# Kernel tuning notes

Measured on AMD Instinct MI355X. Metric: run time of the kernel, lower is better.

The kernel has to match this reference:

```python
import jax, jax.numpy as jnp
import numpy as np


def _jac_det(u):
    # u: [B, 3, D, H, W] displacement field in [-1, 1]-normalized coords
    B, C, D, H, W = u.shape
    scale = jnp.array([(D - 1) / 2.0, (H - 1) / 2.0, (W - 1) / 2.0], dtype=u.dtype)
    phi = u * scale[None, :, None, None, None]
    px, py, pz = phi[:, 0], phi[:, 1], phi[:, 2]  # each [B, D, H, W]
    # torch.gradient == numpy.gradient: central differences interior, one-sided edges
    gx = lambda a: jnp.gradient(a, axis=-3)
    gy = lambda a: jnp.gradient(a, axis=-2)
    gz = lambda a: jnp.gradient(a, axis=-1)
    dxx = gx(px) + 1.0
    dxy = gy(px)
    dxz = gz(px)
    dyx = gx(py)
    dyy = gy(py) + 1.0
    dyz = gz(py)
    dzx = gx(pz)
    dzy = gy(pz)
    dzz = gz(pz) + 1.0
    det = (dxx * (dyy * dzz - dyz * dzy)
           + dxy * (dyz * dzx - dyx * dzz)
           + dxz * (dyx * dzy - dyy * dzx))
    return det


def setup_inputs() -> dict:
    key = jax.random.key(0)
    displacement_field = jax.random.normal(key, (2, 3, 160, 192, 160), dtype=jnp.float32) * 0.05
    return {"displacement_field": displacement_field}


def reference(displacement_field):
    det = _jac_det(displacement_field)
    # loss = mean(relu(-det))
    return jnp.mean(jax.nn.relu(-det))
```

## Files before the change

### kernel.cpp

```cpp
#include <hip/hip_runtime.h>

#define Dd 160
#define Hh 192
#define Ww 160
#define HW (Hh * Ww)
#define DHW ((size_t)Dd * HW)
#define NVOX_D 9830400.0

#define TH 8
#define TD 5
#define QROW (Ww / 4)
#define TPB (QROW * TH)
#define NHT (Hh / TH)
#define NDS (Dd / TD)
#define GRID1 (2 * NHT * NDS)
#define NXCD 8
#define CHUNK (GRID1 / NXCD)
#define NWAVE (TPB / 64)
#define BLK2 512

__device__ __forceinline__ float4 ld4(const float* p) {
    return *reinterpret_cast<const float4*>(p);
}

__device__ __forceinline__ float4 wgrad(float4 cc, float lft, float rgt, int w0) {
    float4 g;
    g.x = (w0 == 0)      ? (cc.y - cc.x) : 0.5f * (cc.y - lft);
    g.y = 0.5f * (cc.z - cc.x);
    g.z = 0.5f * (cc.w - cc.y);
    g.w = (w0 + 4 == Ww) ? (cc.w - cc.z) : 0.5f * (rgt - cc.z);
    return g;
}

__device__ __forceinline__ float relu_negdet(
    float gd0, float gh0, float gw0,
    float gd1, float gh1, float gw1,
    float gd2, float gh2, float gw2)
{
    const float sx = 79.5f;
    const float sy = 95.5f;
    const float sz = 79.5f;
    float dxx = fmaf(sx, gd0, 1.0f);
    float dxy = sx * gh0;
    float dxz = sx * gw0;
    float dyx = sy * gd1;
    float dyy = fmaf(sy, gh1, 1.0f);
    float dyz = sy * gw1;
    float dzx = sz * gd2;
    float dzy = sz * gh2;
    float dzz = fmaf(sz, gw2, 1.0f);
    float det = dxx * (dyy * dzz - dyz * dzy)
              + dxy * (dyz * dzx - dyx * dzz)
              + dxz * (dyx * dzy - dyy * dzx);
    return fmaxf(-det, 0.0f);
}

__global__ __launch_bounds__(TPB) void jac_partial(const float* __restrict__ u,
                                                   float* __restrict__ part)
{
    const int lg  = (blockIdx.x % NXCD) * CHUNK + blockIdx.x / NXCD;
    const int ds  = lg % NDS;
    const int ht  = (lg / NDS) % NHT;
    const int b   = lg / (NDS * NHT);

    const int tid = threadIdx.x;
    const int wq  = tid % QROW;
    const int hh  = tid / QROW;
    const int h   = ht * TH + hh;
    const int w0  = wq * 4;

    const int hm = (h > 0)      ? h - 1 : 0;
    const int hp = (h < Hh - 1) ? h + 1 : Hh - 1;
    const float hinv = 1.0f / (float)(hp - hm);
    const int offm = (hm - h) * Ww;
    const int offp = (hp - h) * Ww;

    const int d0     = ds * TD;
    const int dir    = (ds & 1) ? -1 : 1;
    const int dstart = (dir > 0) ? d0 : d0 + TD - 1;

    const float* pcA = u + (size_t)(b * 3 + 0) * DHW + (size_t)h * Ww + w0;
    const float* pcB = pcA + DHW;
    const float* pcC = pcA + 2 * DHW;

    float4 a0, a1, b0, b1, c0, c1;
    {
        int db = dstart - dir;
        db = (db < 0) ? 0 : ((db > Dd - 1) ? Dd - 1 : db);
        const size_t om = (size_t)db * HW;
        const size_t oc = (size_t)dstart * HW;
        a0 = ld4(pcA + om);  a1 = ld4(pcA + oc);
        b0 = ld4(pcB + om);  b1 = ld4(pcB + oc);
        c0 = ld4(pcC + om);  c1 = ld4(pcC + oc);
    }

    float acc = 0.0f;

    #pragma unroll
    for (int i = 0; i < TD; ++i) {
        const int d  = dstart + dir * i;
        int dn = d + dir;
        dn = (dn < 0) ? 0 : ((dn > Dd - 1) ? Dd - 1 : dn);
        const float dinvs = (float)dir * ((d > 0 && d < Dd - 1) ? 0.5f : 1.0f);
        const size_t od  = (size_t)d  * HW;
        const size_t odn = (size_t)dn * HW;

        float4 a2 = ld4(pcA + odn);
        float4 b2 = ld4(pcB + odn);
        float4 c2 = ld4(pcC + odn);

        const float* pdA = pcA + od;
        const float* pdB = pcB + od;
        const float* pdC = pcC + od;

        float4 rAm = ld4(pdA + offm), rAp = ld4(pdA + offp);
        float4 rBm = ld4(pdB + offm), rBp = ld4(pdB + offp);
        float4 rCm = ld4(pdC + offm), rCp = ld4(pdC + offp);

        float lA = (w0 > 0) ? pdA[-1] : 0.0f;
        float lB = (w0 > 0) ? pdB[-1] : 0.0f;
        float lC = (w0 > 0) ? pdC[-1] : 0.0f;
        float rA = (w0 + 4 < Ww) ? pdA[4] : 0.0f;
        float rB = (w0 + 4 < Ww) ? pdB[4] : 0.0f;
        float rC = (w0 + 4 < Ww) ? pdC[4] : 0.0f;

        float4 gwA = wgrad(a1, lA, rA, w0);
        float4 gwB = wgrad(b1, lB, rB, w0);
        float4 gwC = wgrad(c1, lC, rC, w0);

        float4 ghA = make_float4((rAp.x - rAm.x) * hinv, (rAp.y - rAm.y) * hinv,
                                 (rAp.z - rAm.z) * hinv, (rAp.w - rAm.w) * hinv);
        float4 ghB = make_float4((rBp.x - rBm.x) * hinv, (rBp.y - rBm.y) * hinv,
                                 (rBp.z - rBm.z) * hinv, (rBp.w - rBm.w) * hinv);
        float4 ghC = make_float4((rCp.x - rCm.x) * hinv, (rCp.y - rCm.y) * hinv,
                                 (rCp.z - rCm.z) * hinv, (rCp.w - rCm.w) * hinv);

        float4 gdA = make_float4((a2.x - a0.x) * dinvs, (a2.y - a0.y) * dinvs,
                                 (a2.z - a0.z) * dinvs, (a2.w - a0.w) * dinvs);
        float4 gdB = make_float4((b2.x - b0.x) * dinvs, (b2.y - b0.y) * dinvs,
                                 (b2.z - b0.z) * dinvs, (b2.w - b0.w) * dinvs);
        float4 gdC = make_float4((c2.x - c0.x) * dinvs, (c2.y - c0.y) * dinvs,
                                 (c2.z - c0.z) * dinvs, (c2.w - c0.w) * dinvs);

        acc += relu_negdet(gdA.x, ghA.x, gwA.x, gdB.x, ghB.x, gwB.x, gdC.x, ghC.x, gwC.x)
             + relu_negdet(gdA.y, ghA.y, gwA.y, gdB.y, ghB.y, gwB.y, gdC.y, ghC.y, gwC.y)
             + relu_negdet(gdA.z, ghA.z, gwA.z, gdB.z, ghB.z, gwB.z, gdC.z, ghC.z, gwC.z)
             + relu_negdet(gdA.w, ghA.w, gwA.w, gdB.w, ghB.w, gwB.w, gdC.w, ghC.w, gwC.w);

        a0 = a1; a1 = a2;
        b0 = b1; b1 = b2;
        c0 = c1; c1 = c2;
    }

    #pragma unroll
    for (int off = 32; off > 0; off >>= 1)
        acc += __shfl_down(acc, off, 64);
    __shared__ float sred[NWAVE];
    const int lane = tid & 63;
    const int wid  = tid >> 6;
    if (lane == 0) sred[wid] = acc;
    __syncthreads();
    if (tid == 0)
        part[lg] = ((sred[0] + sred[1]) + (sred[2] + sred[3])) + sred[4];
}

__global__ __launch_bounds__(BLK2) void jac_final(const float* __restrict__ part,
                                                  float* __restrict__ out)
{
    const int t = threadIdx.x;
    double a = (double)part[t] + (double)part[t + 512] + (double)part[t + 1024];
    __shared__ double s[BLK2];
    s[t] = a;
    __syncthreads();
    #pragma unroll
    for (int off = BLK2 / 2; off > 0; off >>= 1) {
        if (t < off) s[t] += s[t + off];
        __syncthreads();
    }
    if (t == 0)
        out[0] = (float)(s[0] / NVOX_D);
}

extern "C" void kernel_launch(void* const* d_in, const int* in_sizes, int n_in,
                              void* d_out, int out_size, void* d_ws, size_t ws_size,
                              hipStream_t stream)
{
    const float* u = (const float*)d_in[0];
    float* part = (float*)d_ws;

    jac_partial<<<GRID1, TPB, 0, stream>>>(u, part);
    jac_final<<<1, BLK2, 0, stream>>>(part, (float*)d_out);
}
```

Baseline: 46.26 us.

## Process two H rows per thread and use wave shuffles for W neighbors

Each thread now handles two adjacent H rows, so the two rows supply each other's H neighbors and fewer loads per output are needed. The per-element left/right W neighbor loads are replaced with wave shuffles, with scalar fallback loads only at wave boundaries. The grid halves, and the final reduction is resized to 768 partials. This raises register pressure (the D loop is now unroll 2, with 3-channel by 2-row arrays) and halves the block count, which may hurt occupancy.

```diff
diff --git a/kernel.cpp b/kernel.cpp
--- a/kernel.cpp
+++ b/kernel.cpp
@@ -7,20 +7,29 @@
 #define DHW ((size_t)Dd * HW)
 #define NVOX_D 9830400.0
 
-#define TH 8
+#define TH 16
 #define TD 5
 #define QROW (Ww / 4)
-#define TPB (QROW * TH)
+#define TPB (QROW * 8)
 #define NHT (Hh / TH)
 #define NDS (Dd / TD)
 #define GRID1 (2 * NHT * NDS)
 #define NXCD 8
 #define CHUNK (GRID1 / NXCD)
 #define NWAVE (TPB / 64)
-#define BLK2 512
+#define BLK2 256
 
 __device__ __forceinline__ float4 ld4(const float* p) {
     return *reinterpret_cast<const float4*>(p);
+}
+
+__device__ __forceinline__ int clampi(int v, int lo, int hi) {
+    return (v < lo) ? lo : ((v > hi) ? hi : v);
+}
+
+__device__ __forceinline__ float4 d4(float4 a, float4 b, float s) {
+    return make_float4((a.x - b.x) * s, (a.y - b.y) * s,
+                       (a.z - b.z) * s, (a.w - b.w) * s);
 }
 
 __device__ __forceinline__ float4 wgrad(float4 cc, float lft, float rgt, int w0) {
@@ -55,6 +64,17 @@
     return fmaxf(-det, 0.0f);
 }
 
+__device__ __forceinline__ float row_dets(
+    float4 gdA, float4 ghA, float4 gwA,
+    float4 gdB, float4 ghB, float4 gwB,
+    float4 gdC, float4 ghC, float4 gwC)
+{
+    return relu_negdet(gdA.x, ghA.x, gwA.x, gdB.x, ghB.x, gwB.x, gdC.x, ghC.x, gwC.x)
+         + relu_negdet(gdA.y, ghA.y, gwA.y, gdB.y, ghB.y, gwB.y, gdC.y, ghC.y, gwC.y)
+         + relu_negdet(gdA.z, ghA.z, gwA.z, gdB.z, ghB.z, gwB.z, gdC.z, ghC.z, gwC.z)
+         + relu_negdet(gdA.w, ghA.w, gwA.w, gdB.w, ghB.w, gwB.w, gdC.w, ghC.w, gwC.w);
+}
+
 __global__ __launch_bounds__(TPB) void jac_partial(const float* __restrict__ u,
                                                    float* __restrict__ part)
 {
@@ -63,101 +83,112 @@
     const int ht  = (lg / NDS) % NHT;
     const int b   = lg / (NDS * NHT);
 
-    const int tid = threadIdx.x;
-    const int wq  = tid % QROW;
-    const int hh  = tid / QROW;
-    const int h   = ht * TH + hh;
-    const int w0  = wq * 4;
-
-    const int hm = (h > 0)      ? h - 1 : 0;
-    const int hp = (h < Hh - 1) ? h + 1 : Hh - 1;
-    const float hinv = 1.0f / (float)(hp - hm);
-    const int offm = (hm - h) * Ww;
-    const int offp = (hp - h) * Ww;
+    const int tid  = threadIdx.x;
+    const int wq   = tid % QROW;
+    const int hg   = tid / QROW;
+    const int h0   = ht * TH + hg * 2;
+    const int h1   = h0 + 1;
+    const int w0   = wq * 4;
+    const int lane = tid & 63;
+
+    const bool fixlo = (lane == 0)  && (wq > 0);
+    const bool fixhi = (lane == 63) && (wq < QROW - 1);
+
+    const float hinv0 = (h0 > 0) ? 0.5f : 1.0f;
+    const float hinv1 = (h1 < Hh - 1) ? 0.5f : 1.0f;
+    const int offm = ((h0 > 0 ? h0 - 1 : 0) - h0) * Ww;
+    const int offp = (((h1 < Hh - 1) ? h1 + 1 : Hh - 1) - h0) * Ww;
 
     const int d0     = ds * TD;
     const int dir    = (ds & 1) ? -1 : 1;
     const int dstart = (dir > 0) ? d0 : d0 + TD - 1;
 
-    const float* pcA = u + (size_t)(b * 3 + 0) * DHW + (size_t)h * Ww + w0;
-    const float* pcB = pcA + DHW;
-    const float* pcC = pcA + 2 * DHW;
-
-    float4 a0, a1, b0, b1, c0, c1;
+    const float* pc[3];
+    pc[0] = u + (size_t)(b * 3 + 0) * DHW + (size_t)h0 * Ww + w0;
+    pc[1] = pc[0] + DHW;
+    pc[2] = pc[0] + 2 * DHW;
+
+    float4 p0[3][2], p1[3][2], p2[3][2];
     {
-        int db = dstart - dir;
-        db = (db < 0) ? 0 : ((db > Dd - 1) ? Dd - 1 : db);
-        const size_t om = (size_t)db * HW;
+        const size_t om = (size_t)clampi(dstart - dir, 0, Dd - 1) * HW;
         const size_t oc = (size_t)dstart * HW;
-        a0 = ld4(pcA + om);  a1 = ld4(pcA + oc);
-        b0 = ld4(pcB + om);  b1 = ld4(pcB + oc);
-        c0 = ld4(pcC + om);  c1 = ld4(pcC + oc);
+        #pragma unroll
+        for (int ch = 0; ch < 3; ++ch) {
+            p0[ch][0] = ld4(pc[ch] + om);       p0[ch][1] = ld4(pc[ch] + om + Ww);
+            p1[ch][0] = ld4(pc[ch] + oc);       p1[ch][1] = ld4(pc[ch] + oc + Ww);
+        }
     }
 
     float acc = 0.0f;
 
-    #pragma unroll
+    #pragma unroll 2
     for (int i = 0; i < TD; ++i) {
         const int d  = dstart + dir * i;
-        int dn = d + dir;
-        dn = (dn < 0) ? 0 : ((dn > Dd - 1) ? Dd - 1 : dn);
+        const int dn = clampi(d + dir, 0, Dd - 1);
         const float dinvs = (float)dir * ((d > 0 && d < Dd - 1) ? 0.5f : 1.0f);
         const size_t od  = (size_t)d  * HW;
         const size_t odn = (size_t)dn * HW;
 
-        float4 a2 = ld4(pcA + odn);
-        float4 b2 = ld4(pcB + odn);
-        float4 c2 = ld4(pcC + odn);
-
-        const float* pdA = pcA + od;
-        const float* pdB = pcB + od;
-        const float* pdC = pcC + od;
-
-        float4 rAm = ld4(pdA + offm), rAp = ld4(pdA + offp);
-        float4 rBm = ld4(pdB + offm), rBp = ld4(pdB + offp);
-        float4 rCm = ld4(pdC + offm), rCp = ld4(pdC + offp);
-
-        float lA = (w0 > 0) ? pdA[-1] : 0.0f;
-        float lB = (w0 > 0) ? pdB[-1] : 0.0f;
-        float lC = (w0 > 0) ? pdC[-1] : 0.0f;
-        float rA = (w0 + 4 < Ww) ? pdA[4] : 0.0f;
-        float rB = (w0 + 4 < Ww) ? pdB[4] : 0.0f;
-        float rC = (w0 + 4 < Ww) ? pdC[4] : 0.0f;
-
-        float4 gwA = wgrad(a1, lA, rA, w0);
-        float4 gwB = wgrad(b1, lB, rB, w0);
-        float4 gwC = wgrad(c1, lC, rC, w0);
-
-        float4 ghA = make_float4((rAp.x - rAm.x) * hinv, (rAp.y - rAm.y) * hinv,
-                                 (rAp.z - rAm.z) * hinv, (rAp.w - rAm.w) * hinv);
-        float4 ghB = make_float4((rBp.x - rBm.x) * hinv, (rBp.y - rBm.y) * hinv,
-                                 (rBp.z - rBm.z) * hinv, (rBp.w - rBm.w) * hinv);
-        float4 ghC = make_float4((rCp.x - rCm.x) * hinv, (rCp.y - rCm.y) * hinv,
-                                 (rCp.z - rCm.z) * hinv, (rCp.w - rCm.w) * hinv);
-
-        float4 gdA = make_float4((a2.x - a0.x) * dinvs, (a2.y - a0.y) * dinvs,
-                                 (a2.z - a0.z) * dinvs, (a2.w - a0.w) * dinvs);
-        float4 gdB = make_float4((b2.x - b0.x) * dinvs, (b2.y - b0.y) * dinvs,
-                                 (b2.z - b0.z) * dinvs, (b2.w - b0.w) * dinvs);
-        float4 gdC = make_float4((c2.x - c0.x) * dinvs, (c2.y - c0.y) * dinvs,
-                                 (c2.z - c0.z) * dinvs, (c2.w - c0.w) * dinvs);
-
-        acc += relu_negdet(gdA.x, ghA.x, gwA.x, gdB.x, ghB.x, gwB.x, gdC.x, ghC.x, gwC.x)
-             + relu_negdet(gdA.y, ghA.y, gwA.y, gdB.y, ghB.y, gwB.y, gdC.y, ghC.y, gwC.y)
-             + relu_negdet(gdA.z, ghA.z, gwA.z, gdB.z, ghB.z, gwB.z, gdC.z, ghC.z, gwC.z)
-             + relu_negdet(gdA.w, ghA.w, gwA.w, gdB.w, ghB.w, gwB.w, gdC.w, ghC.w, gwC.w);
-
-        a0 = a1; a1 = a2;
-        b0 = b1; b1 = b2;
-        c0 = c1; c1 = c2;
+        float4 hm[3], hp[3];
+        #pragma unroll
+        for (int ch = 0; ch < 3; ++ch) {
+            hm[ch]    = ld4(pc[ch] + od + offm);
+            hp[ch]    = ld4(pc[ch] + od + offp);
+            p2[ch][0] = ld4(pc[ch] + odn);
+            p2[ch][1] = ld4(pc[ch] + odn + Ww);
+        }
+        float lf[3][2], rf[3][2];
+        if (fixlo) {
+            #pragma unroll
+            for (int ch = 0; ch < 3; ++ch) {
+                lf[ch][0] = (pc[ch] + od)[-1];
+                lf[ch][1] = (pc[ch] + od + Ww)[-1];
+            }
+        }
+        if (fixhi) {
+            #pragma unroll
+            for (int ch = 0; ch < 3; ++ch) {
+                rf[ch][0] = (pc[ch] + od)[4];
+                rf[ch][1] = (pc[ch] + od + Ww)[4];
+            }
+        }
+
+        float4 gw[3][2], gh[3][2], gd[3][2];
+        #pragma unroll
+        for (int ch = 0; ch < 3; ++ch) {
+            #pragma unroll
+            for (int r = 0; r < 2; ++r) {
+                float4 cc = p1[ch][r];
+                float lft = __shfl_up(cc.w, 1);
+                float rgt = __shfl_down(cc.x, 1);
+                if (fixlo) lft = lf[ch][r];
+                if (fixhi) rgt = rf[ch][r];
+                gw[ch][r] = wgrad(cc, lft, rgt, w0);
+                gd[ch][r] = d4(p2[ch][r], p0[ch][r], dinvs);
+            }
+            gh[ch][0] = d4(p1[ch][1], hm[ch], hinv0);
+            gh[ch][1] = d4(hp[ch], p1[ch][0], hinv1);
+        }
+
+        acc += row_dets(gd[0][0], gh[0][0], gw[0][0],
+                        gd[1][0], gh[1][0], gw[1][0],
+                        gd[2][0], gh[2][0], gw[2][0])
+             + row_dets(gd[0][1], gh[0][1], gw[0][1],
+                        gd[1][1], gh[1][1], gw[1][1],
+                        gd[2][1], gh[2][1], gw[2][1]);
+
+        #pragma unroll
+        for (int ch = 0; ch < 3; ++ch) {
+            p0[ch][0] = p1[ch][0]; p0[ch][1] = p1[ch][1];
+            p1[ch][0] = p2[ch][0]; p1[ch][1] = p2[ch][1];
+        }
     }
 
     #pragma unroll
     for (int off = 32; off > 0; off >>= 1)
         acc += __shfl_down(acc, off, 64);
     __shared__ float sred[NWAVE];
-    const int lane = tid & 63;
-    const int wid  = tid >> 6;
+    const int wid = tid >> 6;
     if (lane == 0) sred[wid] = acc;
     __syncthreads();
     if (tid == 0)
@@ -168,7 +199,7 @@
                                                   float* __restrict__ out)
 {
     const int t = threadIdx.x;
-    double a = (double)part[t] + (double)part[t + 512] + (double)part[t + 1024];
+    double a = (double)part[t] + (double)part[t + 256] + (double)part[t + 512];
     __shared__ double s[BLK2];
     s[t] = a;
     __syncthreads();
```

New measurement: 107.1 us. +131.6%, slower.
